# Kernel tuning notes

Measured on AMD Instinct MI355X. Metric: run time of the kernel, lower is better.

Reference implementation:

```python
import jax, jax.numpy as jnp
import numpy as np

B, S, HID = 1, 2048, 2048
H, HD, DR = 16, 128, 64
CKV, CQ = 512, 1536
ROPE_BASE = 10000.0


def _rope_cos_sin(seq_len, dim, dtype):
    inv_freq = 1.0 / (ROPE_BASE ** (jnp.arange(0, dim, 2, dtype=jnp.float32) / dim))
    t = jnp.arange(seq_len, dtype=jnp.float32)
    freqs = jnp.outer(t, inv_freq)                      # [S, DR/2]
    emb = jnp.concatenate([freqs, freqs], axis=-1)      # [S, DR]
    return jnp.cos(emb).astype(dtype), jnp.sin(emb).astype(dtype)


def _rotate_half(x):
    x1, x2 = jnp.split(x, 2, axis=-1)
    return jnp.concatenate([-x2, x1], axis=-1)


def _xavier(key, fan_in, fan_out):
    lim = np.sqrt(6.0 / (fan_in + fan_out))
    return jax.random.uniform(key, (fan_in, fan_out), jnp.float32, -lim, lim)


def setup_inputs() -> dict:
    key = jax.random.key(0)
    ks = jax.random.split(key, 10)
    hidden_states = jax.random.normal(ks[0], (B, S, HID), jnp.float32)
    # causal mask: 1.0 where position is masked out (j > i)
    mask = jnp.triu(jnp.ones((S, S), jnp.float32), k=1)[None, None]  # [1,1,S,S]
    return {
        "hidden_states": hidden_states,
        "mask": mask,
        "W_DKV": _xavier(ks[1], HID, CKV),
        "W_UK": _xavier(ks[2], CKV, H * HD),
        "W_UV": _xavier(ks[3], CKV, H * HD),
        "W_DQ": _xavier(ks[4], HID, CQ),
        "W_UQ": _xavier(ks[5], CQ, H * HD),
        "W_QR": _xavier(ks[6], CQ, H * DR),
        "W_KR": _xavier(ks[7], HID, DR),
        "W_O": _xavier(ks[8], H * HD, HID),
    }


def reference(hidden_states, mask, W_DKV, W_UK, W_UV, W_DQ, W_UQ, W_QR, W_KR, W_O):
    b, s, _ = hidden_states.shape
    scale = 1.0 / np.sqrt(HD + DR)

    c_KV = hidden_states @ W_DKV                         # [B,S,CKV]
    k_C = (c_KV @ W_UK).reshape(b, s, H, HD)
    v = (c_KV @ W_UV).reshape(b, s, H, HD)
    c_Q = hidden_states @ W_DQ                           # [B,S,CQ]
    q_C = (c_Q @ W_UQ).reshape(b, s, H, HD)
    q_R = (c_Q @ W_QR).reshape(b, s, H, DR)
    k_R = (hidden_states @ W_KR).reshape(b, s, 1, DR)

    cos, sin = _rope_cos_sin(s, DR, hidden_states.dtype)
    cos = cos[None, :, None, :]                          # [1,S,1,DR]
    sin = sin[None, :, None, :]
    q_R = q_R * cos + _rotate_half(q_R) * sin
    k_R = k_R * cos + _rotate_half(k_R) * sin            # [B,S,1,DR], broadcast over heads

    q = jnp.concatenate([q_C, q_R], axis=-1)             # [B,S,H,HD+DR]
    k = jnp.concatenate([k_C, jnp.broadcast_to(k_R, (b, s, H, DR))], axis=-1)

    # [B,H,Sq,Sk]
    scores = jnp.einsum("bqhd,bkhd->bhqk", q, k) * scale
    if mask is not None:
        scores = scores + mask * -1e9                     # broadcast over heads
    probs = jax.nn.softmax(scores, axis=-1)
    out = jnp.einsum("bhqk,bkhd->bqhd", probs, v).reshape(b, s, H * HD)
    return out @ W_O
```

## Files before the change

kernel.cpp:

```cpp
#include <hip/hip_runtime.h>
#include <hip/hip_bf16.h>
#include <math.h>

typedef __hip_bfloat16 bf16;
typedef short s16x8 __attribute__((ext_vector_type(8)));
typedef unsigned short u16x8 __attribute__((ext_vector_type(8)));
typedef float f32x4 __attribute__((ext_vector_type(4)));

#define S_LEN 2048
#define NHEAD 16
#define HDIM  128
#define DROT  64

__device__ __forceinline__ float bf2f(unsigned short u) {
    union { unsigned int i; float f; } v;
    v.i = ((unsigned int)u) << 16;
    return v.f;
}
__device__ __forceinline__ unsigned short f2bf(float f) {
    union { float f; unsigned int i; } v;
    v.f = f;
    unsigned int r = (v.i + 0x7FFFu + ((v.i >> 16) & 1u)) >> 16;
    return (unsigned short)r;
}

__device__ __forceinline__ void load_lds16(const unsigned short* g, unsigned short* l) {
    __builtin_amdgcn_global_load_lds(
        (const __attribute__((address_space(1))) unsigned short*)g,
        (__attribute__((address_space(3))) unsigned short*)l, 16, 0, 0);
}

__device__ __forceinline__ bool is_bf16(const unsigned int* maskw) {
    return maskw[1] != 0x3F800000u;
}

struct PrepDesc {
    const void* in;
    unsigned short* out;
    int R, C, blk_start, nbx, kind;
};
struct PrepBatch { PrepDesc d[8]; };

__global__ __launch_bounds__(256)
void prep_kernel(PrepBatch b, const unsigned int* __restrict__ maskw) {
    const bool fb = is_bf16(maskw);
    __shared__ unsigned short t[64][80];
    PrepDesc dd = b.d[0];
    #pragma unroll
    for (int p = 1; p < 8; ++p)
        if ((int)blockIdx.x >= b.d[p].blk_start) dd = b.d[p];
    const int local = (int)blockIdx.x - dd.blk_start;
    const int tid = threadIdx.x;

    if (dd.kind == 1) {
        const size_t idx = ((size_t)local * 256 + tid) * 8;
        if (fb) {
            *(u16x8*)(dd.out + idx) = *(const u16x8*)((const unsigned short*)dd.in + idx);
        } else {
            const float* p = (const float*)dd.in + idx;
            float4 f0 = *(const float4*)p;
            float4 f1 = *(const float4*)(p + 4);
            u16x8 u;
            u[0] = f2bf(f0.x); u[1] = f2bf(f0.y); u[2] = f2bf(f0.z); u[3] = f2bf(f0.w);
            u[4] = f2bf(f1.x); u[5] = f2bf(f1.y); u[6] = f2bf(f1.z); u[7] = f2bf(f1.w);
            *(u16x8*)(dd.out + idx) = u;
        }
        return;
    }

    const int by = local / dd.nbx, bx = local - by * dd.nbx;
    const int r0 = by << 6, c0 = bx << 6;
    const int tr = tid >> 3;
    const int tc8 = (tid & 7) << 3;
    #pragma unroll
    for (int p = 0; p < 2; ++p) {
        const int r = tr + p * 32;
        const size_t off = (size_t)(r0 + r) * dd.C + c0 + tc8;
        unsigned short v[8];
        if (fb) {
            u16x8 u = *(const u16x8*)((const unsigned short*)dd.in + off);
            #pragma unroll
            for (int j = 0; j < 8; ++j) v[j] = u[j];
        } else {
            const float* p4 = (const float*)dd.in + off;
            float4 f0 = *(const float4*)p4;
            float4 f1 = *(const float4*)(p4 + 4);
            v[0] = f2bf(f0.x); v[1] = f2bf(f0.y); v[2] = f2bf(f0.z); v[3] = f2bf(f0.w);
            v[4] = f2bf(f1.x); v[5] = f2bf(f1.y); v[6] = f2bf(f1.z); v[7] = f2bf(f1.w);
        }
        #pragma unroll
        for (int j = 0; j < 8; ++j) t[tc8 + j][r] = v[j];
    }
    __syncthreads();
    #pragma unroll
    for (int p = 0; p < 2; ++p) {
        const int c = tr + p * 32;
        u16x8 u = *(const u16x8*)&t[c][tc8];
        *(u16x8*)(dd.out + (size_t)(c0 + c) * dd.R + r0 + tc8) = u;
    }
}

__global__ __launch_bounds__(256)
void transpose_conv(const void* __restrict__ in, unsigned short* __restrict__ out,
                    int R, int C, const unsigned int* __restrict__ maskw) {
    const bool fb = is_bf16(maskw);
    __shared__ unsigned short t[64][80];
    const int r0 = blockIdx.y << 6, c0 = blockIdx.x << 6;
    const int tid = threadIdx.x;
    const int tr = tid >> 3;
    const int tc8 = (tid & 7) << 3;
    #pragma unroll
    for (int p = 0; p < 2; ++p) {
        const int r = tr + p * 32;
        const size_t off = (size_t)(r0 + r) * C + c0 + tc8;
        unsigned short v[8];
        if (fb) {
            u16x8 u = *(const u16x8*)((const unsigned short*)in + off);
            #pragma unroll
            for (int j = 0; j < 8; ++j) v[j] = u[j];
        } else {
            const float* p4 = (const float*)in + off;
            float4 f0 = *(const float4*)p4;
            float4 f1 = *(const float4*)(p4 + 4);
            v[0] = f2bf(f0.x); v[1] = f2bf(f0.y); v[2] = f2bf(f0.z); v[3] = f2bf(f0.w);
            v[4] = f2bf(f1.x); v[5] = f2bf(f1.y); v[6] = f2bf(f1.z); v[7] = f2bf(f1.w);
        }
        #pragma unroll
        for (int j = 0; j < 8; ++j) t[tc8 + j][r] = v[j];
    }
    __syncthreads();
    #pragma unroll
    for (int p = 0; p < 2; ++p) {
        const int c = tr + p * 32;
        u16x8 u = *(const u16x8*)&t[c][tc8];
        *(u16x8*)(out + (size_t)(c0 + c) * R + r0 + tc8) = u;
    }
}

struct GemmDesc {
    const unsigned short* A;
    const unsigned short* Bt;
    void* C;
    int M, N, K;
    int nbx;
    int blk_start;
    int ct;
};
struct GemmBatch { GemmDesc d[4]; };

template <int NP, int CMODE>
__global__ __launch_bounds__(256)
void mfma_gemm2(GemmBatch batch, const unsigned int* __restrict__ maskw) {
    __shared__ __align__(16) unsigned short As[2][128 * 64];
    __shared__ __align__(16) unsigned short Bs[2][64 * 64];

    GemmDesc dd = batch.d[0];
    #pragma unroll
    for (int p = 1; p < NP; ++p)
        if ((int)blockIdx.x >= batch.d[p].blk_start) dd = batch.d[p];
    const int local = (int)blockIdx.x - dd.blk_start;
    const int by = local / dd.nbx;
    const int bx = local - by * dd.nbx;
    const int m0 = by << 7, n0 = bx << 6;
    const int K = dd.K;

    const int tid  = threadIdx.x;
    const int lane = tid & 63;
    const int w    = tid >> 6;
    const int wr = w >> 1, wc = w & 1;
    const int l15 = lane & 15, quad = lane >> 4, q8 = quad << 3;

    int arow[4], acol[4], adst[4];
    #pragma unroll
    for (int i = 0; i < 4; ++i) {
        const int c = 4 * w + i;
        const int sl = c >> 3, sub = c & 7;
        arow[i] = sub * 16 + (lane >> 2);
        acol[i] = sl * 32 + (lane & 3) * 8;
        adst[i] = sl * 4096 + sub * 512 + lane * 8;
    }
    int brow[2], bcol[2], bdst[2];
    #pragma unroll
    for (int i = 0; i < 2; ++i) {
        const int c = 2 * w + i;
        const int sl = c >> 2, sub = c & 3;
        brow[i] = sub * 16 + (lane >> 2);
        bcol[i] = sl * 32 + (lane & 3) * 8;
        bdst[i] = sl * 2048 + sub * 512 + lane * 8;
    }

    f32x4 acc[4][2];
    #pragma unroll
    for (int i = 0; i < 4; ++i)
        #pragma unroll
        for (int j = 0; j < 2; ++j) {
            f32x4 z = {0.f, 0.f, 0.f, 0.f};
            acc[i][j] = z;
        }

    #pragma unroll
    for (int i = 0; i < 4; ++i)
        load_lds16(dd.A + (size_t)(m0 + arow[i]) * K + acol[i], As[0] + adst[i]);
    #pragma unroll
    for (int i = 0; i < 2; ++i)
        load_lds16(dd.Bt + (size_t)(n0 + brow[i]) * K + bcol[i], Bs[0] + bdst[i]);
    __syncthreads();

    int cur = 0;
    for (int k0 = 0; k0 < K; k0 += 64) {
        if (k0 + 64 < K) {
            #pragma unroll
            for (int i = 0; i < 4; ++i)
                load_lds16(dd.A + (size_t)(m0 + arow[i]) * K + k0 + 64 + acol[i],
                           As[cur ^ 1] + adst[i]);
            #pragma unroll
            for (int i = 0; i < 2; ++i)
                load_lds16(dd.Bt + (size_t)(n0 + brow[i]) * K + k0 + 64 + bcol[i],
                           Bs[cur ^ 1] + bdst[i]);
        }
        s16x8 af[4][2], bf[2][2];
        #pragma unroll
        for (int mt = 0; mt < 4; ++mt)
            #pragma unroll
            for (int ks = 0; ks < 2; ++ks)
                af[mt][ks] = *(const s16x8*)&As[cur][ks * 4096 + (wr * 64 + mt * 16 + l15) * 32 + q8];
        #pragma unroll
        for (int nt = 0; nt < 2; ++nt)
            #pragma unroll
            for (int ks = 0; ks < 2; ++ks)
                bf[nt][ks] = *(const s16x8*)&Bs[cur][ks * 2048 + (wc * 32 + nt * 16 + l15) * 32 + q8];
        #pragma unroll
        for (int ks = 0; ks < 2; ++ks)
            #pragma unroll
            for (int nt = 0; nt < 2; ++nt)
                #pragma unroll
                for (int mt = 0; mt < 4; ++mt)
                    acc[mt][nt] = __builtin_amdgcn_mfma_f32_16x16x32_bf16(
                        af[mt][ks], bf[nt][ks], acc[mt][nt], 0, 0, 0);
        __syncthreads();
        cur ^= 1;
    }

    bool cbf = true;
    if (CMODE == 2) cbf = is_bf16(maskw);
    const int M = dd.M, N = dd.N;
    #pragma unroll
    for (int mt = 0; mt < 4; ++mt)
        #pragma unroll
        for (int nt = 0; nt < 2; ++nt) {
            f32x4 d = acc[mt][nt];
            const int col  = n0 + wc * 32 + nt * 16 + l15;
            const int rowb = m0 + wr * 64 + mt * 16 + quad * 4;
            if (dd.ct) {
                ushort4 o;
                o.x = f2bf(d[0]); o.y = f2bf(d[1]); o.z = f2bf(d[2]); o.w = f2bf(d[3]);
                *(ushort4*)((unsigned short*)dd.C + (size_t)col * M + rowb) = o;
            } else if (cbf) {
                unsigned short* c = (unsigned short*)dd.C + (size_t)rowb * N + col;
                #pragma unroll
                for (int r = 0; r < 4; ++r) c[(size_t)r * N] = f2bf(d[r]);
            } else {
                float* c = (float*)dd.C + (size_t)rowb * N + col;
                #pragma unroll
                for (int r = 0; r < 4; ++r) c[(size_t)r * N] = d[r];
            }
        }
}

__global__ __launch_bounds__(256)
void rope_all(unsigned short* __restrict__ qR, unsigned short* __restrict__ kRb) {
    int bid = blockIdx.x;
    unsigned short* x;
    int nh, stride;
    if (bid < 4096) { x = qR; nh = 16; stride = 64; }
    else            { x = kRb; nh = 1; stride = 128; bid -= 4096; }
    const int idx = bid * 256 + threadIdx.x;
    const int d = idx & 31;
    const int rest = idx >> 5;
    const int h = rest % nh;
    const int s = rest / nh;
    if (s >= S_LEN) return;
    const float inv = powf(10000.0f, -(float)d * (1.0f / 32.0f));
    const float ang = (float)s * inv;
    float si, co;
    sincosf(ang, &si, &co);
    unsigned short* p = x + ((size_t)s * nh + h) * stride;
    const float x1 = bf2f(p[d]);
    const float x2 = bf2f(p[d + 32]);
    p[d]      = f2bf(x1 * co - x2 * si);
    p[d + 32] = f2bf(x2 * co + x1 * si);
}

__global__ __launch_bounds__(512)
void mfma_attn(const unsigned short* __restrict__ qC,
               const unsigned short* __restrict__ qR,
               const unsigned short* __restrict__ kC,
               const unsigned short* __restrict__ kRb,
               const unsigned short* __restrict__ vT,
               unsigned short* __restrict__ at) {
    __shared__ __align__(16) union {
        struct {
            unsigned short Ks[64][200];
            unsigned short Vs[128][72];
            unsigned short Ps[8][16][40];
        } s;
        struct {
            float O[4][16][132];
            float L[4][16];
        } m;
    } sm;

    const int tid  = threadIdx.x;
    const int lane = tid & 63;
    const int w    = tid >> 6;
    const int qs   = w & 3;
    const int kh   = w >> 2;
    const int l15 = lane & 15, quad = lane >> 4, q8 = quad << 3;

    const int bid   = (int)blockIdx.x;
    const int h     = bid & 15;
    const int qbase = bid >> 4;

    const float scale = 0.0721687836487032f;

    const int krow = tid >> 3;
    const int kcb  = (tid & 7) * 24;
    const int vd   = tid >> 2;
    const int vcb  = (tid & 3) << 4;

    #pragma unroll
    for (int part = 0; part < 2; ++part) {
        const int qb = part ? (31 - qbase) : qbase;
        const int q0 = qb << 6;
        const int qrow0 = q0 + qs * 16;

        s16x8 qf[6];
        {
            const int qrow = qrow0 + l15;
            const unsigned short* qCrow = qC + ((size_t)qrow * NHEAD + h) * HDIM;
            #pragma unroll
            for (int s = 0; s < 4; ++s)
                qf[s] = *(const s16x8*)(qCrow + s * 32 + q8);
            const unsigned short* qRrow = qR + ((size_t)qrow * NHEAD + h) * DROT;
            #pragma unroll
            for (int s = 0; s < 2; ++s)
                qf[4 + s] = *(const s16x8*)(qRrow + s * 32 + q8);
        }

        f32x4 accO[8];
        #pragma unroll
        for (int i = 0; i < 8; ++i) { f32x4 z = {0.f, 0.f, 0.f, 0.f}; accO[i] = z; }
        float slocal[4] = {0.f, 0.f, 0.f, 0.f};

        const int ntiles = (q0 >> 6) + 1;

        u16x8 kreg[3], vreg[2];
        {
            #pragma unroll
            for (int m = 0; m < 3; ++m) {
                const int c = kcb + m * 8;
                const unsigned short* src = (c < 128)
                    ? kC + ((size_t)krow * NHEAD + h) * HDIM + c
                    : kRb + (size_t)krow * 128 + (c - 128);
                kreg[m] = *(const u16x8*)src;
            }
            const unsigned short* vrow = vT + (size_t)(h * HDIM + vd) * S_LEN;
            #pragma unroll
            for (int m = 0; m < 2; ++m)
                vreg[m] = *(const u16x8*)(vrow + vcb + m * 8);
        }

        for (int t = 0; t < ntiles; ++t) {
            const int key0 = t << 6;
            __syncthreads();
            #pragma unroll
            for (int m = 0; m < 3; ++m)
                *(u16x8*)&sm.s.Ks[krow][kcb + m * 8] = kreg[m];
            #pragma unroll
            for (int m = 0; m < 2; ++m)
                *(u16x8*)&sm.s.Vs[vd][vcb + m * 8] = vreg[m];
            __syncthreads();

            if (t + 1 < ntiles) {
                const int kn = key0 + 64;
                #pragma unroll
                for (int m = 0; m < 3; ++m) {
                    const int c = kcb + m * 8;
                    const unsigned short* src = (c < 128)
                        ? kC + ((size_t)(kn + krow) * NHEAD + h) * HDIM + c
                        : kRb + (size_t)(kn + krow) * 128 + (c - 128);
                    kreg[m] = *(const u16x8*)src;
                }
                const unsigned short* vrow = vT + (size_t)(h * HDIM + vd) * S_LEN + kn;
                #pragma unroll
                for (int m = 0; m < 2; ++m)
                    vreg[m] = *(const u16x8*)(vrow + vcb + m * 8);
            }

            const int wk0 = key0 + kh * 32;
            const bool active = wk0 <= qrow0 + 15;
            if (active) {
                f32x4 sA[2];
                #pragma unroll
                for (int nt = 0; nt < 2; ++nt) { f32x4 z = {0.f, 0.f, 0.f, 0.f}; sA[nt] = z; }
                #pragma unroll
                for (int s = 0; s < 6; ++s)
                    #pragma unroll
                    for (int nt = 0; nt < 2; ++nt) {
                        s16x8 kf = *(const s16x8*)&sm.s.Ks[kh * 32 + nt * 16 + l15][s * 32 + q8];
                        sA[nt] = __builtin_amdgcn_mfma_f32_16x16x32_bf16(qf[s], kf, sA[nt], 0, 0, 0);
                    }

                const int rbase = qrow0 + quad * 4;
                const bool diag = (wk0 + 31 > qrow0);
                #pragma unroll
                for (int nt = 0; nt < 2; ++nt) {
                    const int col = wk0 + nt * 16 + l15;
                    #pragma unroll
                    for (int r = 0; r < 4; ++r) {
                        float s = sA[nt][r] * scale;
                        if (diag && (col > rbase + r)) s = -1e30f;
                        const float p = __expf(s);
                        slocal[r] += p;
                        sm.s.Ps[w][quad * 4 + r][nt * 16 + l15] = f2bf(p);
                    }
                }

                s16x8 pf = *(const s16x8*)&sm.s.Ps[w][l15][q8];
                #pragma unroll
                for (int dt = 0; dt < 8; ++dt) {
                    s16x8 vf = *(const s16x8*)&sm.s.Vs[dt * 16 + l15][kh * 32 + q8];
                    accO[dt] = __builtin_amdgcn_mfma_f32_16x16x32_bf16(pf, vf, accO[dt], 0, 0, 0);
                }
            }
        }

        float l_r[4];
        #pragma unroll
        for (int r = 0; r < 4; ++r) {
            float sum = slocal[r];
            #pragma unroll
            for (int off = 1; off < 16; off <<= 1)
                sum += __shfl_xor(sum, off, 64);
            l_r[r] = sum;
        }

        __syncthreads();
        if (kh == 1) {
            #pragma unroll
            for (int dt = 0; dt < 8; ++dt)
                #pragma unroll
                for (int r = 0; r < 4; ++r)
                    sm.m.O[qs][quad * 4 + r][dt * 16 + l15] = accO[dt][r];
            if (l15 == 0)
                #pragma unroll
                for (int r = 0; r < 4; ++r)
                    sm.m.L[qs][quad * 4 + r] = l_r[r];
        }
        __syncthreads();
        if (kh == 0) {
            float linv[4];
            #pragma unroll
            for (int r = 0; r < 4; ++r)
                linv[r] = 1.f / (l_r[r] + sm.m.L[qs][quad * 4 + r]);
            #pragma unroll
            for (int r = 0; r < 4; ++r) {
                const int row = qrow0 + quad * 4 + r;
                unsigned short* dst = at + (size_t)row * (NHEAD * HDIM) + h * HDIM + l15;
                #pragma unroll
                for (int dt = 0; dt < 8; ++dt) {
                    const float o = accO[dt][r]
                                  + sm.m.O[qs][quad * 4 + r][dt * 16 + l15];
                    dst[dt * 16] = f2bf(o * linv[r]);
                }
            }
        }
    }
}

extern "C" void kernel_launch(void* const* d_in, const int* in_sizes, int n_in,
                              void* d_out, int out_size, void* d_ws, size_t ws_size,
                              hipStream_t stream) {
    (void)in_sizes; (void)n_in; (void)out_size; (void)ws_size;

    const void* hs    = d_in[0];
    const unsigned int* maskw = (const unsigned int*)d_in[1];
    const void* W_DKV = d_in[2];
    const void* W_UK  = d_in[3];
    const void* W_UV  = d_in[4];
    const void* W_DQ  = d_in[5];
    const void* W_UQ  = d_in[6];
    const void* W_QR  = d_in[7];
    const void* W_KR  = d_in[8];
    const void* W_O   = d_in[9];

    const size_t M1 = 1048576;
    unsigned short* ws    = (unsigned short*)d_ws;
    unsigned short* cKV   = ws;
    unsigned short* cQ    = ws + 1 * M1;
    unsigned short* kC    = ws + 4 * M1;
    unsigned short* vT    = ws + 8 * M1;
    unsigned short* DKVt  = ws + 8 * M1;
    unsigned short* DQt   = ws + 9 * M1;
    unsigned short* qC    = ws + 12 * M1;
    unsigned short* hs_bf = ws + 12 * M1;
    unsigned short* qR    = ws + 16 * M1;
    unsigned short* kRb   = ws + 18 * M1;
    unsigned short* KRt   = ws + 18 * M1 + 262144;
    unsigned short* at    = ws + 18 * M1 + 524288;
    unsigned short* UKt   = at;
    unsigned short* UVt   = at + 1 * M1;
    unsigned short* QRt   = at + 2 * M1;
    unsigned short* UQt   = ws + 22 * M1 + 524288;
    unsigned short* WOt   = ws;

    const dim3 blk(256);

    {
        PrepBatch b{};
        b.d[0] = { hs,    hs_bf, 0, 0,           0,  0, 1 };
        b.d[1] = { W_DKV, DKVt,  2048,  512,  2048,  8, 0 };
        b.d[2] = { W_DQ,  DQt,   2048, 1536,  2304, 24, 0 };
        b.d[3] = { W_KR,  KRt,   2048,   64,  3072,  1, 0 };
        b.d[4] = { W_UK,  UKt,    512, 2048,  3104, 32, 0 };
        b.d[5] = { W_UV,  UVt,    512, 2048,  3360, 32, 0 };
        b.d[6] = { W_UQ,  UQt,   1536, 2048,  3616, 32, 0 };
        b.d[7] = { W_QR,  QRt,   1536, 1024,  4384, 16, 0 };
        prep_kernel<<<4768, blk, 0, stream>>>(b, maskw);
    }

    {
        GemmBatch b{};
        b.d[0] = { hs_bf, DQt,  (void*)cQ,  2048, 1536, 2048, 24,   0, 0 };
        b.d[1] = { hs_bf, DKVt, (void*)cKV, 2048,  512, 2048,  8, 384, 0 };
        b.d[2] = { hs_bf, KRt,  (void*)kRb, 2048,  128, 2048,  2, 512, 0 };
        b.d[3] = b.d[2];
        mfma_gemm2<3, 1><<<544, blk, 0, stream>>>(b, maskw);
    }

    {
        GemmBatch b{};
        b.d[0] = { cQ,  UQt, (void*)qC, 2048, 2048, 1536, 32,    0, 0 };
        b.d[1] = { cQ,  QRt, (void*)qR, 2048, 1024, 1536, 16,  512, 0 };
        b.d[2] = { cKV, UKt, (void*)kC, 2048, 2048,  512, 32,  768, 0 };
        b.d[3] = { cKV, UVt, (void*)vT, 2048, 2048,  512, 32, 1280, 1 };
        mfma_gemm2<4, 1><<<1792, blk, 0, stream>>>(b, maskw);
    }

    rope_all<<<4352, blk, 0, stream>>>(qR, kRb);

    transpose_conv<<<dim3(32, 32), blk, 0, stream>>>(W_O, WOt, 2048, 2048, maskw);

    mfma_attn<<<256, dim3(512), 0, stream>>>(qC, qR, kC, kRb, vT, at);

    {
        GemmBatch b{};
        b.d[0] = { at, WOt, d_out, 2048, 2048, 2048, 32, 0, 0 };
        b.d[1] = b.d[0]; b.d[2] = b.d[0]; b.d[3] = b.d[0];
        mfma_gemm2<1, 2><<<512, blk, 0, stream>>>(b, maskw);
    }
}
```

Baseline: 305.2 us.

## Process both paired query tiles concurrently with 32-row warp tiles and direct V loads

Each block previously handled two causally paired query tiles one after another. Now half the warps take each tile and share a single K tile loop. Each warp now covers 32 query rows (two MFMA row tiles), so every K and V fragment is reused twice. V is read straight from global/L2 instead of being staged in LDS, which removes the V shared buffer and its stores. The costs are higher register pressure, warps on the shorter tile sitting idle in later iterations, and uncoalesced global V loads inside the inner loop.

```diff
diff --git a/kernel.cpp b/kernel.cpp
--- a/kernel.cpp
+++ b/kernel.cpp
@@ -301,180 +301,195 @@
     __shared__ __align__(16) union {
         struct {
             unsigned short Ks[64][200];
-            unsigned short Vs[128][72];
-            unsigned short Ps[8][16][40];
+            unsigned short Ps[8][32][40];
         } s;
         struct {
-            float O[4][16][132];
-            float L[4][16];
+            float O[2][32][132];
+            float L[2][32];
         } m;
     } sm;
 
     const int tid  = threadIdx.x;
     const int lane = tid & 63;
     const int w    = tid >> 6;
-    const int qs   = w & 3;
-    const int kh   = w >> 2;
+    const int Tw   = w >> 2;
+    const int qh   = (w >> 1) & 1;
+    const int kh   = w & 1;
     const int l15 = lane & 15, quad = lane >> 4, q8 = quad << 3;
 
     const int bid   = (int)blockIdx.x;
     const int h     = bid & 15;
     const int qbase = bid >> 4;
 
+    const int qbW = Tw ? (31 - qbase) : qbase;
+    const int q0w = qbW << 6;
+    const int qrow0 = q0w + qh * 32;
+    const int ntilesW = qbW + 1;
+    const int ntiles  = 32 - qbase;
+
     const float scale = 0.0721687836487032f;
+
+    s16x8 qf[2][6];
+    #pragma unroll
+    for (int mt = 0; mt < 2; ++mt) {
+        const int qrow = qrow0 + mt * 16 + l15;
+        const unsigned short* qCrow = qC + ((size_t)qrow * NHEAD + h) * HDIM;
+        #pragma unroll
+        for (int s = 0; s < 4; ++s)
+            qf[mt][s] = *(const s16x8*)(qCrow + s * 32 + q8);
+        const unsigned short* qRrow = qR + ((size_t)qrow * NHEAD + h) * DROT;
+        #pragma unroll
+        for (int s = 0; s < 2; ++s)
+            qf[mt][4 + s] = *(const s16x8*)(qRrow + s * 32 + q8);
+    }
+
+    f32x4 accO[2][8];
+    #pragma unroll
+    for (int mt = 0; mt < 2; ++mt)
+        #pragma unroll
+        for (int i = 0; i < 8; ++i) { f32x4 z = {0.f, 0.f, 0.f, 0.f}; accO[mt][i] = z; }
+    float slocal[2][4] = {{0.f, 0.f, 0.f, 0.f}, {0.f, 0.f, 0.f, 0.f}};
 
     const int krow = tid >> 3;
     const int kcb  = (tid & 7) * 24;
-    const int vd   = tid >> 2;
-    const int vcb  = (tid & 3) << 4;
-
-    #pragma unroll
-    for (int part = 0; part < 2; ++part) {
-        const int qb = part ? (31 - qbase) : qbase;
-        const int q0 = qb << 6;
-        const int qrow0 = q0 + qs * 16;
-
-        s16x8 qf[6];
-        {
-            const int qrow = qrow0 + l15;
-            const unsigned short* qCrow = qC + ((size_t)qrow * NHEAD + h) * HDIM;
-            #pragma unroll
-            for (int s = 0; s < 4; ++s)
-                qf[s] = *(const s16x8*)(qCrow + s * 32 + q8);
-            const unsigned short* qRrow = qR + ((size_t)qrow * NHEAD + h) * DROT;
-            #pragma unroll
-            for (int s = 0; s < 2; ++s)
-                qf[4 + s] = *(const s16x8*)(qRrow + s * 32 + q8);
-        }
-
-        f32x4 accO[8];
-        #pragma unroll
-        for (int i = 0; i < 8; ++i) { f32x4 z = {0.f, 0.f, 0.f, 0.f}; accO[i] = z; }
-        float slocal[4] = {0.f, 0.f, 0.f, 0.f};
-
-        const int ntiles = (q0 >> 6) + 1;
-
-        u16x8 kreg[3], vreg[2];
-        {
+
+    u16x8 kreg[3];
+    {
+        #pragma unroll
+        for (int m = 0; m < 3; ++m) {
+            const int c = kcb + m * 8;
+            const unsigned short* src = (c < 128)
+                ? kC + ((size_t)krow * NHEAD + h) * HDIM + c
+                : kRb + (size_t)krow * 128 + (c - 128);
+            kreg[m] = *(const u16x8*)src;
+        }
+    }
+
+    const unsigned short* vbase = vT + (size_t)h * HDIM * S_LEN;
+
+    for (int t = 0; t < ntiles; ++t) {
+        const int key0 = t << 6;
+        __syncthreads();
+        #pragma unroll
+        for (int m = 0; m < 3; ++m)
+            *(u16x8*)&sm.s.Ks[krow][kcb + m * 8] = kreg[m];
+        __syncthreads();
+
+        if (t + 1 < ntiles) {
+            const int kn = key0 + 64;
             #pragma unroll
             for (int m = 0; m < 3; ++m) {
                 const int c = kcb + m * 8;
                 const unsigned short* src = (c < 128)
-                    ? kC + ((size_t)krow * NHEAD + h) * HDIM + c
-                    : kRb + (size_t)krow * 128 + (c - 128);
+                    ? kC + ((size_t)(kn + krow) * NHEAD + h) * HDIM + c
+                    : kRb + (size_t)(kn + krow) * 128 + (c - 128);
                 kreg[m] = *(const u16x8*)src;
             }
-            const unsigned short* vrow = vT + (size_t)(h * HDIM + vd) * S_LEN;
-            #pragma unroll
-            for (int m = 0; m < 2; ++m)
-                vreg[m] = *(const u16x8*)(vrow + vcb + m * 8);
-        }
-
-        for (int t = 0; t < ntiles; ++t) {
-            const int key0 = t << 6;
-            __syncthreads();
-            #pragma unroll
-            for (int m = 0; m < 3; ++m)
-                *(u16x8*)&sm.s.Ks[krow][kcb + m * 8] = kreg[m];
-            #pragma unroll
-            for (int m = 0; m < 2; ++m)
-                *(u16x8*)&sm.s.Vs[vd][vcb + m * 8] = vreg[m];
-            __syncthreads();
-
-            if (t + 1 < ntiles) {
-                const int kn = key0 + 64;
-                #pragma unroll
-                for (int m = 0; m < 3; ++m) {
-                    const int c = kcb + m * 8;
-                    const unsigned short* src = (c < 128)
-                        ? kC + ((size_t)(kn + krow) * NHEAD + h) * HDIM + c
-                        : kRb + (size_t)(kn + krow) * 128 + (c - 128);
-                    kreg[m] = *(const u16x8*)src;
+        }
+
+        const int wk0 = key0 + kh * 32;
+        const bool active = (t < ntilesW) && (wk0 <= qrow0 + 31);
+        if (active) {
+            f32x4 sA[2][2];
+            #pragma unroll
+            for (int mt = 0; mt < 2; ++mt)
+                #pragma unroll
+                for (int nt = 0; nt < 2; ++nt) { f32x4 z = {0.f, 0.f, 0.f, 0.f}; sA[mt][nt] = z; }
+            #pragma unroll
+            for (int s = 0; s < 6; ++s)
+                #pragma unroll
+                for (int nt = 0; nt < 2; ++nt) {
+                    s16x8 kf = *(const s16x8*)&sm.s.Ks[kh * 32 + nt * 16 + l15][s * 32 + q8];
+                    #pragma unroll
+                    for (int mt = 0; mt < 2; ++mt)
+                        sA[mt][nt] = __builtin_amdgcn_mfma_f32_16x16x32_bf16(
+                            qf[mt][s], kf, sA[mt][nt], 0, 0, 0);
                 }
-                const unsigned short* vrow = vT + (size_t)(h * HDIM + vd) * S_LEN + kn;
-                #pragma unroll
-                for (int m = 0; m < 2; ++m)
-                    vreg[m] = *(const u16x8*)(vrow + vcb + m * 8);
-            }
-
-            const int wk0 = key0 + kh * 32;
-            const bool active = wk0 <= qrow0 + 15;
-            if (active) {
-                f32x4 sA[2];
-                #pragma unroll
-                for (int nt = 0; nt < 2; ++nt) { f32x4 z = {0.f, 0.f, 0.f, 0.f}; sA[nt] = z; }
-                #pragma unroll
-                for (int s = 0; s < 6; ++s)
-                    #pragma unroll
-                    for (int nt = 0; nt < 2; ++nt) {
-                        s16x8 kf = *(const s16x8*)&sm.s.Ks[kh * 32 + nt * 16 + l15][s * 32 + q8];
-                        sA[nt] = __builtin_amdgcn_mfma_f32_16x16x32_bf16(qf[s], kf, sA[nt], 0, 0, 0);
-                    }
-
-                const int rbase = qrow0 + quad * 4;
-                const bool diag = (wk0 + 31 > qrow0);
+
+            #pragma unroll
+            for (int mt = 0; mt < 2; ++mt) {
+                const int rbase = qrow0 + mt * 16 + quad * 4;
+                const bool diag = (wk0 + 31 > qrow0 + mt * 16);
                 #pragma unroll
                 for (int nt = 0; nt < 2; ++nt) {
                     const int col = wk0 + nt * 16 + l15;
                     #pragma unroll
                     for (int r = 0; r < 4; ++r) {
-                        float s = sA[nt][r] * scale;
-                        if (diag && (col > rbase + r)) s = -1e30f;
-                        const float p = __expf(s);
-                        slocal[r] += p;
-                        sm.s.Ps[w][quad * 4 + r][nt * 16 + l15] = f2bf(p);
+                        float sv = sA[mt][nt][r] * scale;
+                        if (diag && (col > rbase + r)) sv = -1e30f;
+                        const float p = __expf(sv);
+                        slocal[mt][r] += p;
+                        sm.s.Ps[w][mt * 16 + quad * 4 + r][nt * 16 + l15] = f2bf(p);
                     }
                 }
-
-                s16x8 pf = *(const s16x8*)&sm.s.Ps[w][l15][q8];
-                #pragma unroll
-                for (int dt = 0; dt < 8; ++dt) {
-                    s16x8 vf = *(const s16x8*)&sm.s.Vs[dt * 16 + l15][kh * 32 + q8];
-                    accO[dt] = __builtin_amdgcn_mfma_f32_16x16x32_bf16(pf, vf, accO[dt], 0, 0, 0);
+            }
+
+            s16x8 pf[2];
+            #pragma unroll
+            for (int mt = 0; mt < 2; ++mt)
+                pf[mt] = *(const s16x8*)&sm.s.Ps[w][mt * 16 + l15][q8];
+            #pragma unroll
+            for (int dt = 0; dt < 8; ++dt) {
+                s16x8 vf = *(const s16x8*)(vbase + (size_t)(dt * 16 + l15) * S_LEN + wk0 + q8);
+                #pragma unroll
+                for (int mt = 0; mt < 2; ++mt)
+                    accO[mt][dt] = __builtin_amdgcn_mfma_f32_16x16x32_bf16(
+                        pf[mt], vf, accO[mt][dt], 0, 0, 0);
+            }
+        }
+    }
+
+    float l_r[2][4];
+    #pragma unroll
+    for (int mt = 0; mt < 2; ++mt)
+        #pragma unroll
+        for (int r = 0; r < 4; ++r) {
+            float sum = slocal[mt][r];
+            #pragma unroll
+            for (int off = 1; off < 16; off <<= 1)
+                sum += __shfl_xor(sum, off, 64);
+            l_r[mt][r] = sum;
+        }
+
+    __syncthreads();
+    #pragma unroll
+    for (int ph = 0; ph < 2; ++ph) {
+        if (Tw == ph && kh == 1) {
+            #pragma unroll
+            for (int mt = 0; mt < 2; ++mt) {
+                #pragma unroll
+                for (int dt = 0; dt < 8; ++dt)
+                    #pragma unroll
+                    for (int r = 0; r < 4; ++r)
+                        sm.m.O[qh][mt * 16 + quad * 4 + r][dt * 16 + l15] = accO[mt][dt][r];
+                if (l15 == 0)
+                    #pragma unroll
+                    for (int r = 0; r < 4; ++r)
+                        sm.m.L[qh][mt * 16 + quad * 4 + r] = l_r[mt][r];
+            }
+        }
+        __syncthreads();
+        if (Tw == ph && kh == 0) {
+            #pragma unroll
+            for (int mt = 0; mt < 2; ++mt) {
+                float linv[4];
+                #pragma unroll
+                for (int r = 0; r < 4; ++r)
+                    linv[r] = 1.f / (l_r[mt][r] + sm.m.L[qh][mt * 16 + quad * 4 + r]);
+                #pragma unroll
+                for (int r = 0; r < 4; ++r) {
+                    const int row = qrow0 + mt * 16 + quad * 4 + r;
+                    unsigned short* dst = at + (size_t)row * (NHEAD * HDIM) + h * HDIM + l15;
+                    #pragma unroll
+                    for (int dt = 0; dt < 8; ++dt) {
+                        const float o = accO[mt][dt][r]
+                                      + sm.m.O[qh][mt * 16 + quad * 4 + r][dt * 16 + l15];
+                        dst[dt * 16] = f2bf(o * linv[r]);
+                    }
                 }
             }
         }
-
-        float l_r[4];
-        #pragma unroll
-        for (int r = 0; r < 4; ++r) {
-            float sum = slocal[r];
-            #pragma unroll
-            for (int off = 1; off < 16; off <<= 1)
-                sum += __shfl_xor(sum, off, 64);
-            l_r[r] = sum;
-        }
-
         __syncthreads();
-        if (kh == 1) {
-            #pragma unroll
-            for (int dt = 0; dt < 8; ++dt)
-                #pragma unroll
-                for (int r = 0; r < 4; ++r)
-                    sm.m.O[qs][quad * 4 + r][dt * 16 + l15] = accO[dt][r];
-            if (l15 == 0)
-                #pragma unroll
-                for (int r = 0; r < 4; ++r)
-                    sm.m.L[qs][quad * 4 + r] = l_r[r];
-        }
-        __syncthreads();
-        if (kh == 0) {
-            float linv[4];
-            #pragma unroll
-            for (int r = 0; r < 4; ++r)
-                linv[r] = 1.f / (l_r[r] + sm.m.L[qs][quad * 4 + r]);
-            #pragma unroll
-            for (int r = 0; r < 4; ++r) {
-                const int row = qrow0 + quad * 4 + r;
-                unsigned short* dst = at + (size_t)row * (NHEAD * HDIM) + h * HDIM + l15;
-                #pragma unroll
-                for (int dt = 0; dt < 8; ++dt) {
-                    const float o = accO[dt][r]
-                                  + sm.m.O[qs][quad * 4 + r][dt * 16 + l15];
-                    dst[dt * 16] = f2bf(o * linv[r]);
-                }
-            }
-        }
     }
 }
 
```

New measurement: 330.1 us. 8.2% more time.
